# Optimization experiments

Hardware: AMD Instinct MI355X
Metric: run time of the kernel (lower is better)

Reference implementation:

```python
import jax, jax.numpy as jnp
import numpy as np
from jax import lax

G = 8  # number of RBF grid points (FastKAN default style)
GRID = jnp.linspace(-2.0, 2.0, G)
DENOM = 4.0 / (G - 1)  # grid spacing used as gaussian width


def _fastkan_conv(x, ln_w, ln_b, Wb, bb, Ws):
    # x: [B, C, H, W]; 3x3 conv, stride 1, pad 1 via patch unfold + FastKAN linear
    B, C, H, W = x.shape
    p = lax.conv_general_dilated_patches(x, (3, 3), (1, 1), ((1, 1), (1, 1)))  # [B, C*9, H, W]
    p = p.transpose(0, 2, 3, 1).reshape(B * H * W, C * 9)  # [N, in]
    # LayerNorm over patch features (FastKAN normalizes before the RBF basis)
    mu = p.mean(-1, keepdims=True)
    var = p.var(-1, keepdims=True)
    pn = (p - mu) / jnp.sqrt(var + 1e-5) * ln_w + ln_b
    # Gaussian RBF basis: [N, in, G]
    rbf = jnp.exp(-jnp.square((pn[:, :, None] - GRID) / DENOM))
    spline = rbf.reshape(B * H * W, -1) @ Ws.T          # [N, out]
    base = jax.nn.silu(p) @ Wb.T + bb                    # [N, out]
    out = spline + base
    return out.reshape(B, H, W, -1).transpose(0, 3, 1, 2)  # [B, out, H, W]


def _bn_relu_pool(h, gamma, beta):
    # BatchNorm2d in training mode (batch stats), ReLU, MaxPool2d(2,2)
    mu = h.mean((0, 2, 3), keepdims=True)
    var = h.var((0, 2, 3), keepdims=True)
    h = (h - mu) / jnp.sqrt(var + 1e-5) * gamma[None, :, None, None] + beta[None, :, None, None]
    h = jax.nn.relu(h)
    return lax.reduce_window(h, -jnp.inf, lax.max, (1, 1, 2, 2), (1, 1, 2, 2), 'VALID')


def setup_inputs() -> dict:
    key = jax.random.key(0)
    ks = jax.random.split(key, 16)
    B, Cin, H, W = 32, 16, 64, 64
    dims = [(Cin * 9, 64), (64 * 9, 128), (128 * 9, 256)]
    inp = {"x": jax.random.normal(ks[0], (B, Cin, H, W), jnp.float32)}
    for i, (fin, fout) in enumerate(dims, 1):
        inp[f"ln_w{i}"] = jnp.ones((fin,), jnp.float32)
        inp[f"ln_b{i}"] = jnp.zeros((fin,), jnp.float32)
        inp[f"Wb{i}"] = jax.random.normal(ks[3 * i], (fout, fin), jnp.float32) * 0.05
        inp[f"bb{i}"] = jnp.zeros((fout,), jnp.float32)
        inp[f"Ws{i}"] = jax.random.normal(ks[3 * i + 1], (fout, fin * G), jnp.float32) * 0.05
        inp[f"g{i}"] = jnp.ones((fout,), jnp.float32)
        inp[f"be{i}"] = jnp.zeros((fout,), jnp.float32)
    return inp


def reference(x, ln_w1, ln_b1, Wb1, bb1, Ws1, g1, be1,
              ln_w2, ln_b2, Wb2, bb2, Ws2, g2, be2,
              ln_w3, ln_b3, Wb3, bb3, Ws3, g3, be3):
    h = _bn_relu_pool(_fastkan_conv(x, ln_w1, ln_b1, Wb1, bb1, Ws1), g1, be1)
    h = _bn_relu_pool(_fastkan_conv(h, ln_w2, ln_b2, Wb2, bb2, Ws2), g2, be2)
    h = _bn_relu_pool(_fastkan_conv(h, ln_w3, ln_b3, Wb3, bb3, Ws3), g3, be3)
    return h.reshape(h.shape[0], -1)  # flatten: [B, 256*8*8]
```

## Files before the change

kernel.cpp:

```cpp
#include <hip/hip_runtime.h>

typedef _Float16 half_t;
typedef __attribute__((ext_vector_type(8))) _Float16 half8;
typedef __attribute__((ext_vector_type(4))) float floatx4;


#define RBF_SCALE 2.1019644f
#define RBF_G0   -4.2039288f
#define RBF_2D    2.40224482f
#define RBF_D2    1.44269504f
#define RBF_Q     0.13533528f

template<int C, int H, int W>
__global__ __launch_bounds__(256)
void ln_prep(const float* __restrict__ x,
             const float* __restrict__ lnw, const float* __restrict__ lnb,
             half_t* __restrict__ pn, half_t* __restrict__ sp)
{
    const int HW = H * W, IN = C * 9;
    const int NL = (IN + 63) / 64;
    const int wv = threadIdx.x >> 6, lane = threadIdx.x & 63;
    const int pix = blockIdx.x * 4 + wv;
    const int b = pix / HW, hw = pix % HW, h = hw / W, w = hw % W;
    const float* xb = x + (long)b * C * HW;

    float v[NL];
    float s = 0.f, s2 = 0.f;
    #pragma unroll
    for (int t = 0; t < NL; ++t) {
        int i = t * 64 + lane;
        float val = 0.f;
        if (i < IN) {
            int ch = i / 9, r = i - ch * 9;
            int y = h + r / 3 - 1, xx = w + r % 3 - 1;
            if (y >= 0 && y < H && xx >= 0 && xx < W)
                val = xb[ch * HW + y * W + xx];
        }
        v[t] = val; s += val; s2 += val * val;
    }
    #pragma unroll
    for (int off = 32; off > 0; off >>= 1) {
        s  += __shfl_down(s,  off, 64);
        s2 += __shfl_down(s2, off, 64);
    }
    s = __shfl(s, 0, 64); s2 = __shfl(s2, 0, 64);
    float mean = s / IN;
    float istd = rsqrtf(s2 / IN - mean * mean + 1e-5f);

    #pragma unroll
    for (int t = 0; t < NL; ++t) {
        int i = t * 64 + lane;
        if (i < IN) {
            float val = v[t];
            float pnv = (val - mean) * istd * lnw[i] + lnb[i];
            pnv = fminf(12.f, fmaxf(-12.f, pnv * RBF_SCALE));
            pn[(long)pix * IN + i] = (half_t)pnv;
            sp[(long)pix * IN + i] = (half_t)(val / (1.f + __expf(-val)));
        }
    }
}

template<int IN, int OUT>
__global__ __launch_bounds__(256)
void conv_w(const float* __restrict__ Ws, const float* __restrict__ Wb,
            half_t* __restrict__ Wt)
{
    const int NIB = (IN + 63) / 64, NSTEP = NIB * 9;
    int idx = blockIdx.x * 256 + threadIdx.x;
    if (idx >= OUT * NSTEP * 64) return;
    int uu = idx & 63;
    int t = idx >> 6;
    int o = t % OUT;
    int s = t / OUT;
    int iblk = s / 9, j = s % 9;
    int ulin = (((uu >> 3) ^ (o & 7)) << 3) + (uu & 7);
    int i = iblk * 64 + ulin;
    float v = 0.f;
    if (i < IN)
        v = (j < 8) ? Ws[(long)o * IN * 8 + i * 8 + j] : Wb[(long)o * IN + i];
    Wt[idx] = (half_t)v;
}

template<int IN, int OUT, int HW, int NB, int SPLIT>
__global__ __launch_bounds__(256)
void kan_gemm(const half_t* __restrict__ pn, const half_t* __restrict__ sp,
              const half_t* __restrict__ Wt, float* __restrict__ out)
{
    const int NIB = (IN + 63) / 64;

    __shared__ half_t As[64 * 64];
    __shared__ half_t Bs[NB * 64 * 64];

    const int tid = threadIdx.x;
    const int row = tid >> 2, q = tid & 3;
    const int pix = blockIdx.x * 64 + row;
    const half_t* pnrow = pn + (long)pix * IN;
    const half_t* sprow = sp + (long)pix * IN;

    const int wv = tid >> 6, lane = tid & 63;
    const int lr = lane & 15, lq = lane >> 4;
    const int u0 = (2 * q) ^ (row & 7);
    const int u1 = (2 * q + 1) ^ (row & 7);

    floatx4 acc[NB][4] = {};
    float r[16], u[16];

    const int grpA = (blockIdx.z * NIB) / SPLIT;
    const int grpB = ((blockIdx.z + 1) * NIB) / SPLIT;

    int j = 0, iblk = grpA;
    for (int it = grpA * 9; it < grpB * 9; ++it) {
        __syncthreads();

        {
            const half_t* ws = Wt + (long)it * OUT * 64 + wv * (NB * 2 * 512);
            #pragma unroll
            for (int c = 0; c < NB * 2; ++c) {
                __builtin_amdgcn_global_load_lds(
                    (const __attribute__((address_space(1))) void*)(ws + c * 512 + lane * 8),
                    (__attribute__((address_space(3))) void*)(&Bs[wv * (NB * 2 * 512) + c * 512]),
                    16, 0, 0);
            }
        }

        {
            const int i0 = iblk * 64 + q * 16;
            const bool ok = (i0 < IN);
            if (j < 8) {
                if (j == 0) {
                    const half_t* pp = pnrow + (ok ? i0 : 0);
                    half8 p0 = *(const half8*)pp;
                    half8 p1 = *(const half8*)(pp + 8);
                    #pragma unroll
                    for (int kk = 0; kk < 8; ++kk) {
                        float t0 = (float)p0[kk], t1 = (float)p1[kk];
                        float d0 = t0 - RBF_G0, d1 = t1 - RBF_G0;
                        r[kk]     = ok ? __builtin_amdgcn_exp2f(-(d0 * d0)) : 0.f;
                        u[kk]     = ok ? __builtin_amdgcn_exp2f(fmaf(RBF_2D, d0, -RBF_D2)) : 0.f;
                        r[kk + 8] = ok ? __builtin_amdgcn_exp2f(-(d1 * d1)) : 0.f;
                        u[kk + 8] = ok ? __builtin_amdgcn_exp2f(fmaf(RBF_2D, d1, -RBF_D2)) : 0.f;
                    }
                }
                half8 a0, a1;
                #pragma unroll
                for (int kk = 0; kk < 8; ++kk) {
                    a0[kk] = (half_t)r[kk];
                    a1[kk] = (half_t)r[kk + 8];
                }
                *(half8*)&As[row * 64 + u0 * 8] = a0;
                *(half8*)&As[row * 64 + u1 * 8] = a1;
                if (j < 7) {
                    #pragma unroll
                    for (int kk = 0; kk < 16; ++kk) { r[kk] *= u[kk]; u[kk] *= RBF_Q; }
                }
            } else {
                half8 a0 = half8{}, a1 = half8{};
                if (ok) {
                    a0 = *(const half8*)(sprow + i0);
                    a1 = *(const half8*)(sprow + i0 + 8);
                }
                *(half8*)&As[row * 64 + u0 * 8] = a0;
                *(half8*)&As[row * 64 + u1 * 8] = a1;
            }
        }
        __syncthreads();

        __builtin_amdgcn_s_setprio(1);
        #pragma unroll
        for (int ks = 0; ks < 2; ++ks) {
            half8 af[4], bf[NB];
            #pragma unroll
            for (int mf = 0; mf < 4; ++mf) {
                int rr = mf * 16 + lr;
                af[mf] = *(const half8*)&As[rr * 64 + (((ks * 4 + lq) ^ (rr & 7)) * 8)];
            }
            #pragma unroll
            for (int nb = 0; nb < NB; ++nb) {
                int rr = wv * NB * 16 + nb * 16 + lr;
                bf[nb] = *(const half8*)&Bs[rr * 64 + (((ks * 4 + lq) ^ (rr & 7)) * 8)];
            }
            #pragma unroll
            for (int nb = 0; nb < NB; ++nb)
                #pragma unroll
                for (int mf = 0; mf < 4; ++mf)
                    acc[nb][mf] = __builtin_amdgcn_mfma_f32_16x16x32_f16(
                        bf[nb], af[mf], acc[nb][mf], 0, 0, 0);
        }
        __builtin_amdgcn_s_setprio(0);

        if (++j == 9) { j = 0; ++iblk; }
    }

    const long zoff = (long)blockIdx.z * ((long)gridDim.x * 64) * OUT;
    #pragma unroll
    for (int nb = 0; nb < NB; ++nb)
    #pragma unroll
    for (int mf = 0; mf < 4; ++mf)
    #pragma unroll
    for (int reg = 0; reg < 4; ++reg) {
        int o  = wv * NB * 16 + nb * 16 + lq * 4 + reg;
        int p2 = blockIdx.x * 64 + mf * 16 + lr;
        int b2 = p2 / HW, hw2 = p2 % HW;
        out[zoff + ((long)b2 * OUT + o) * HW + hw2] = acc[nb][mf][reg];
    }
}

__launch_bounds__(256)
__global__ void bn_stats(const float* __restrict__ h, const float* __restrict__ bias,
                         int C, int HW, int B, int nz, float* __restrict__ sums)
{
    int c = blockIdx.y;
    float bbc = bias[c];
    long zstride = (long)B * C * HW;
    int total = B * HW;
    float s = 0.f, s2 = 0.f;
    for (int idx = blockIdx.x * 256 + threadIdx.x; idx < total; idx += 256 * gridDim.x) {
        int b = idx / HW, r = idx % HW;
        long base = ((long)b * C + c) * HW + r;
        float v = bbc;
        for (int z = 0; z < nz; ++z) v += h[z * zstride + base];
        s += v; s2 += v * v;
    }
    for (int off = 32; off > 0; off >>= 1) {
        s  += __shfl_down(s,  off, 64);
        s2 += __shfl_down(s2, off, 64);
    }
    __shared__ float rs[4], rs2[4];
    int lane = threadIdx.x & 63, wid = threadIdx.x >> 6;
    if (lane == 0) { rs[wid] = s; rs2[wid] = s2; }
    __syncthreads();
    if (threadIdx.x == 0) {
        atomicAdd(&sums[c],     rs[0] + rs[1] + rs[2] + rs[3]);
        atomicAdd(&sums[C + c], rs2[0] + rs2[1] + rs2[2] + rs2[3]);
    }
}

__launch_bounds__(256)
__global__ void bn_relu_pool(const float* __restrict__ h, const float* __restrict__ sums,
                             const float* __restrict__ bias,
                             const float* __restrict__ gamma, const float* __restrict__ beta,
                             float* __restrict__ out, int B, int C, int H, int W, int nz)
{
    int Ho = H / 2, Wo = W / 2;
    long total = (long)B * C * Ho * Wo;
    long idx = (long)blockIdx.x * 256 + threadIdx.x;
    if (idx >= total) return;
    int pw = idx % Wo; long t = idx / Wo;
    int ph = t % Ho; t /= Ho;
    int c = t % C; int b = (int)(t / C);

    float M = (float)B * H * W;
    float mean = sums[c] / M;
    float var  = sums[C + c] / M - mean * mean;
    float scale = gamma[c] * rsqrtf(var + 1e-5f);
    float shift = beta[c] - mean * scale + bias[c] * scale;

    long zstride = (long)B * C * H * W;
    const float* hp = h + ((long)b * C + c) * H * W;
    float m = 0.f;
    #pragma unroll
    for (int i = 0; i < 2; ++i)
        #pragma unroll
        for (int j = 0; j < 2; ++j) {
            long off = (2 * ph + i) * W + 2 * pw + j;
            float v = 0.f;
            for (int z = 0; z < nz; ++z) v += hp[z * zstride + off];
            v = v * scale + shift;
            m = fmaxf(m, v);
        }
    out[idx] = m;
}

extern "C" void kernel_launch(void* const* d_in, const int* in_sizes, int n_in,
                              void* d_out, int out_size, void* d_ws, size_t ws_size,
                              hipStream_t stream) {
    const float* x     = (const float*)d_in[0];
    const float* ln_w1 = (const float*)d_in[1];  const float* ln_b1 = (const float*)d_in[2];
    const float* Wb1   = (const float*)d_in[3];  const float* bb1   = (const float*)d_in[4];
    const float* Ws1   = (const float*)d_in[5];  const float* g1    = (const float*)d_in[6];
    const float* be1   = (const float*)d_in[7];
    const float* ln_w2 = (const float*)d_in[8];  const float* ln_b2 = (const float*)d_in[9];
    const float* Wb2   = (const float*)d_in[10]; const float* bb2   = (const float*)d_in[11];
    const float* Ws2   = (const float*)d_in[12]; const float* g2    = (const float*)d_in[13];
    const float* be2   = (const float*)d_in[14];
    const float* ln_w3 = (const float*)d_in[15]; const float* ln_b3 = (const float*)d_in[16];
    const float* Wb3   = (const float*)d_in[17]; const float* bb3   = (const float*)d_in[18];
    const float* Ws3   = (const float*)d_in[19]; const float* g3    = (const float*)d_in[20];
    const float* be3   = (const float*)d_in[21];

    const int B = 32;
    char* ws = (char*)d_ws;
    float*  convbuf = (float*)(ws + 0);
    float*  poolbuf = (float*)(ws + 33554432);
    float*  stats1  = (float*)(ws + 41943040);
    float*  stats2  = (float*)(ws + 41945088);
    float*  stats3  = (float*)(ws + 41947136);
    half_t* wt1     = (half_t*)(ws + 41949184);
    half_t* wt2     = (half_t*)(ws + 42170368);
    half_t* wt3     = (half_t*)(ws + 43497472);
    half_t* pnbuf   = (half_t*)(ws + 48805888);
    half_t* spbuf   = (half_t*)(ws + 86554624);

    hipMemsetAsync(stats1, 0, 6144, stream);

    conv_w<144, 64><<<(64 * 27 * 64 + 255) / 256, 256, 0, stream>>>(Ws1, Wb1, wt1);
    conv_w<576, 128><<<(128 * 81 * 64 + 255) / 256, 256, 0, stream>>>(Ws2, Wb2, wt2);
    conv_w<1152, 256><<<(256 * 162 * 64 + 255) / 256, 256, 0, stream>>>(Ws3, Wb3, wt3);

    {
        const int H = 64, W = 64, OUT = 64;
        int npix = B * H * W;
        ln_prep<16, H, W><<<npix / 4, 256, 0, stream>>>(x, ln_w1, ln_b1, pnbuf, spbuf);
        kan_gemm<144, OUT, H * W, 1, 1><<<dim3(npix / 64, 1, 1), 256, 0, stream>>>(
            pnbuf, spbuf, wt1, convbuf);
        bn_stats<<<dim3(64, OUT), 256, 0, stream>>>(convbuf, bb1, OUT, H * W, B, 1, stats1);
        long tot = (long)B * OUT * (H / 2) * (W / 2);
        bn_relu_pool<<<(tot + 255) / 256, 256, 0, stream>>>(
            convbuf, stats1, bb1, g1, be1, poolbuf, B, OUT, H, W, 1);
    }
    {
        const int H = 32, W = 32, OUT = 128;
        int npix = B * H * W;
        ln_prep<64, H, W><<<npix / 4, 256, 0, stream>>>(poolbuf, ln_w2, ln_b2, pnbuf, spbuf);
        kan_gemm<576, OUT, H * W, 2, 2><<<dim3(npix / 64, 1, 2), 256, 0, stream>>>(
            pnbuf, spbuf, wt2, convbuf);
        bn_stats<<<dim3(16, OUT), 256, 0, stream>>>(convbuf, bb2, OUT, H * W, B, 2, stats2);
        long tot = (long)B * OUT * (H / 2) * (W / 2);
        bn_relu_pool<<<(tot + 255) / 256, 256, 0, stream>>>(
            convbuf, stats2, bb2, g2, be2, poolbuf, B, OUT, H, W, 2);
    }
    {
        const int H = 16, W = 16, OUT = 256;
        int npix = B * H * W;
        ln_prep<128, H, W><<<npix / 4, 256, 0, stream>>>(poolbuf, ln_w3, ln_b3, pnbuf, spbuf);
        kan_gemm<1152, OUT, H * W, 4, 4><<<dim3(npix / 64, 1, 4), 256, 0, stream>>>(
            pnbuf, spbuf, wt3, convbuf);
        bn_stats<<<dim3(8, OUT), 256, 0, stream>>>(convbuf, bb3, OUT, H * W, B, 4, stats3);
        long tot = (long)B * OUT * (H / 2) * (W / 2);
        bn_relu_pool<<<(tot + 255) / 256, 256, 0, stream>>>(
            convbuf, stats3, bb3, g3, be3, (float*)d_out, B, OUT, H, W, 4);
    }
}
```

Baseline: 493.1 us.

## Double-buffer LDS tiles in KAN GEMM and split layer-3 output channels across grid y

The GEMM kernel now uses two LDS buffers for A and B. It stages the next iteration's weight tile and generates the next RBF A-tile while MFMAs run on the current buffer, which cuts the per-iteration sync count from two to one. It also adds a blockIdx.y output-channel offset so layer 3 runs with NB=2 and two y-blocks instead of NB=4, doubling the block count. This doubles LDS use, which may lower occupancy, and the A-tile generation now runs alongside MFMA issue.

```diff
diff --git a/kernel.cpp b/kernel.cpp
--- a/kernel.cpp
+++ b/kernel.cpp
@@ -88,8 +88,8 @@
 {
     const int NIB = (IN + 63) / 64;
 
-    __shared__ half_t As[64 * 64];
-    __shared__ half_t Bs[NB * 64 * 64];
+    __shared__ half_t As[2][64 * 64];
+    __shared__ half_t Bs[2][NB * 64 * 64];
 
     const int tid = threadIdx.x;
     const int row = tid >> 2, q = tid & 3;
@@ -101,70 +101,72 @@
     const int lr = lane & 15, lq = lane >> 4;
     const int u0 = (2 * q) ^ (row & 7);
     const int u1 = (2 * q + 1) ^ (row & 7);
+    const int yoff = blockIdx.y * (4 * NB * 16);
 
     floatx4 acc[NB][4] = {};
     float r[16], u[16];
 
     const int grpA = (blockIdx.z * NIB) / SPLIT;
     const int grpB = ((blockIdx.z + 1) * NIB) / SPLIT;
-
-    int j = 0, iblk = grpA;
-    for (int it = grpA * 9; it < grpB * 9; ++it) {
-        __syncthreads();
-
-        {
-            const half_t* ws = Wt + (long)it * OUT * 64 + wv * (NB * 2 * 512);
-            #pragma unroll
-            for (int c = 0; c < NB * 2; ++c) {
-                __builtin_amdgcn_global_load_lds(
-                    (const __attribute__((address_space(1))) void*)(ws + c * 512 + lane * 8),
-                    (__attribute__((address_space(3))) void*)(&Bs[wv * (NB * 2 * 512) + c * 512]),
-                    16, 0, 0);
-            }
-        }
-
-        {
-            const int i0 = iblk * 64 + q * 16;
-            const bool ok = (i0 < IN);
-            if (j < 8) {
-                if (j == 0) {
-                    const half_t* pp = pnrow + (ok ? i0 : 0);
-                    half8 p0 = *(const half8*)pp;
-                    half8 p1 = *(const half8*)(pp + 8);
-                    #pragma unroll
-                    for (int kk = 0; kk < 8; ++kk) {
-                        float t0 = (float)p0[kk], t1 = (float)p1[kk];
-                        float d0 = t0 - RBF_G0, d1 = t1 - RBF_G0;
-                        r[kk]     = ok ? __builtin_amdgcn_exp2f(-(d0 * d0)) : 0.f;
-                        u[kk]     = ok ? __builtin_amdgcn_exp2f(fmaf(RBF_2D, d0, -RBF_D2)) : 0.f;
-                        r[kk + 8] = ok ? __builtin_amdgcn_exp2f(-(d1 * d1)) : 0.f;
-                        u[kk + 8] = ok ? __builtin_amdgcn_exp2f(fmaf(RBF_2D, d1, -RBF_D2)) : 0.f;
-                    }
-                }
-                half8 a0, a1;
+    const int s0 = grpA * 9, s1 = grpB * 9;
+
+    int jg = 0, ibg = grpA;
+
+    auto stageB = [&](int it, int buf) {
+        const half_t* wsrc = Wt + (long)it * OUT * 64
+                              + (long)(yoff + wv * NB * 16) * 64;
+        #pragma unroll
+        for (int c = 0; c < NB * 2; ++c) {
+            __builtin_amdgcn_global_load_lds(
+                (const __attribute__((address_space(1))) void*)(wsrc + c * 512 + lane * 8),
+                (__attribute__((address_space(3))) void*)(&Bs[buf][wv * NB * 1024 + c * 512]),
+                16, 0, 0);
+        }
+    };
+
+    auto genA = [&](int buf) {
+        const int i0 = ibg * 64 + q * 16;
+        const bool ok = (i0 < IN);
+        if (jg < 8) {
+            if (jg == 0) {
+                const half_t* pp = pnrow + (ok ? i0 : 0);
+                half8 p0 = *(const half8*)pp;
+                half8 p1 = *(const half8*)(pp + 8);
                 #pragma unroll
                 for (int kk = 0; kk < 8; ++kk) {
-                    a0[kk] = (half_t)r[kk];
-                    a1[kk] = (half_t)r[kk + 8];
+                    float t0 = (float)p0[kk], t1 = (float)p1[kk];
+                    float d0 = t0 - RBF_G0, d1 = t1 - RBF_G0;
+                    r[kk]     = ok ? __builtin_amdgcn_exp2f(-(d0 * d0)) : 0.f;
+                    u[kk]     = ok ? __builtin_amdgcn_exp2f(fmaf(RBF_2D, d0, -RBF_D2)) : 0.f;
+                    r[kk + 8] = ok ? __builtin_amdgcn_exp2f(-(d1 * d1)) : 0.f;
+                    u[kk + 8] = ok ? __builtin_amdgcn_exp2f(fmaf(RBF_2D, d1, -RBF_D2)) : 0.f;
                 }
-                *(half8*)&As[row * 64 + u0 * 8] = a0;
-                *(half8*)&As[row * 64 + u1 * 8] = a1;
-                if (j < 7) {
-                    #pragma unroll
-                    for (int kk = 0; kk < 16; ++kk) { r[kk] *= u[kk]; u[kk] *= RBF_Q; }
-                }
-            } else {
-                half8 a0 = half8{}, a1 = half8{};
-                if (ok) {
-                    a0 = *(const half8*)(sprow + i0);
-                    a1 = *(const half8*)(sprow + i0 + 8);
-                }
-                *(half8*)&As[row * 64 + u0 * 8] = a0;
-                *(half8*)&As[row * 64 + u1 * 8] = a1;
-            }
-        }
-        __syncthreads();
-
+            }
+            half8 a0, a1;
+            #pragma unroll
+            for (int kk = 0; kk < 8; ++kk) {
+                a0[kk] = (half_t)r[kk];
+                a1[kk] = (half_t)r[kk + 8];
+            }
+            *(half8*)&As[buf][row * 64 + u0 * 8] = a0;
+            *(half8*)&As[buf][row * 64 + u1 * 8] = a1;
+            if (jg < 7) {
+                #pragma unroll
+                for (int kk = 0; kk < 16; ++kk) { r[kk] *= u[kk]; u[kk] *= RBF_Q; }
+            }
+        } else {
+            half8 a0 = half8{}, a1 = half8{};
+            if (ok) {
+                a0 = *(const half8*)(sprow + i0);
+                a1 = *(const half8*)(sprow + i0 + 8);
+            }
+            *(half8*)&As[buf][row * 64 + u0 * 8] = a0;
+            *(half8*)&As[buf][row * 64 + u1 * 8] = a1;
+        }
+        if (++jg == 9) { jg = 0; ++ibg; }
+    };
+
+    auto domfma = [&](int buf) {
         __builtin_amdgcn_s_setprio(1);
         #pragma unroll
         for (int ks = 0; ks < 2; ++ks) {
@@ -172,12 +174,12 @@
             #pragma unroll
             for (int mf = 0; mf < 4; ++mf) {
                 int rr = mf * 16 + lr;
-                af[mf] = *(const half8*)&As[rr * 64 + (((ks * 4 + lq) ^ (rr & 7)) * 8)];
+                af[mf] = *(const half8*)&As[buf][rr * 64 + (((ks * 4 + lq) ^ (rr & 7)) * 8)];
             }
             #pragma unroll
             for (int nb = 0; nb < NB; ++nb) {
                 int rr = wv * NB * 16 + nb * 16 + lr;
-                bf[nb] = *(const half8*)&Bs[rr * 64 + (((ks * 4 + lq) ^ (rr & 7)) * 8)];
+                bf[nb] = *(const half8*)&Bs[buf][rr * 64 + (((ks * 4 + lq) ^ (rr & 7)) * 8)];
             }
             #pragma unroll
             for (int nb = 0; nb < NB; ++nb)
@@ -187,8 +189,20 @@
                         bf[nb], af[mf], acc[nb][mf], 0, 0, 0);
         }
         __builtin_amdgcn_s_setprio(0);
-
-        if (++j == 9) { j = 0; ++iblk; }
+    };
+
+    stageB(s0, 0);
+    genA(0);
+    __syncthreads();
+
+    for (int it = s0; it < s1; ++it) {
+        const int cur = (it - s0) & 1, nxt = cur ^ 1;
+        if (it + 1 < s1) {
+            stageB(it + 1, nxt);
+            genA(nxt);
+        }
+        domfma(cur);
+        __syncthreads();
     }
 
     const long zoff = (long)blockIdx.z * ((long)gridDim.x * 64) * OUT;
@@ -198,7 +212,7 @@
     for (int mf = 0; mf < 4; ++mf)
     #pragma unroll
     for (int reg = 0; reg < 4; ++reg) {
-        int o  = wv * NB * 16 + nb * 16 + lq * 4 + reg;
+        int o  = yoff + wv * NB * 16 + nb * 16 + lq * 4 + reg;
         int p2 = blockIdx.x * 64 + mf * 16 + lr;
         int b2 = p2 / HW, hw2 = p2 % HW;
         out[zoff + ((long)b2 * OUT + o) * HW + hw2] = acc[nb][mf][reg];
@@ -333,7 +347,7 @@
         const int H = 16, W = 16, OUT = 256;
         int npix = B * H * W;
         ln_prep<128, H, W><<<npix / 4, 256, 0, stream>>>(poolbuf, ln_w3, ln_b3, pnbuf, spbuf);
-        kan_gemm<1152, OUT, H * W, 4, 4><<<dim3(npix / 64, 1, 4), 256, 0, stream>>>(
+        kan_gemm<1152, OUT, H * W, 2, 4><<<dim3(npix / 64, 2, 4), 256, 0, stream>>>(
             pnbuf, spbuf, wt3, convbuf);
         bn_stats<<<dim3(8, OUT), 256, 0, stream>>>(convbuf, bb3, OUT, H * W, B, 4, stats3);
         long tot = (long)B * OUT * (H / 2) * (W / 2);
```

New measurement: 512.5 us. +3.9%, slower.
